# Optimization experiments

Hardware: AMD Instinct MI355X
Metric: run time of the kernel (lower is better)

## Reference

```python
import jax, jax.numpy as jnp
import numpy as np

BINS = 100
ALPHA = 0.1

def entropy_batch(h):
    # Faithful to torch: histogram path is detached (done in numpy in original).
    h = jax.lax.stop_gradient(h)
    B, D = h.shape
    hp = h - jnp.min(h, axis=1, keepdims=True)
    hn = hp / jnp.max(hp, axis=1, keepdims=True)  # normalized to [0, 1]
    # np.histogram with `bins` uniform bins over [0,1]; rightmost edge inclusive -> clip
    idx = jnp.clip(jnp.floor(hn * BINS).astype(jnp.int32), 0, BINS - 1)
    rows = jnp.arange(B)[:, None]
    counts = jnp.zeros((B, BINS), jnp.float32).at[rows, idx].add(1.0)
    px = counts / jnp.float32(D)
    safe = jnp.where(px > 0, px, 1.0)
    ent = -jnp.sum(px * jnp.log(safe), axis=1) + jnp.log(jnp.float32(BINS))
    return jnp.mean(ent)

def setup_inputs() -> dict:
    key = jax.random.key(0)
    ks = jax.random.split(key, 8)
    B = 65536
    archi = [246, 246, 246, 246, 246, 246]
    dims = [784] + archi
    inp = {"x": jax.random.normal(ks[0], (B, 1, 28, 28), jnp.float32)}
    for i in range(6):
        inp[f"W{i+1}"] = 0.01 * jax.random.normal(ks[i + 1], (dims[i + 1], dims[i]), jnp.float32)
        inp[f"b{i+1}"] = jnp.zeros((dims[i + 1],), jnp.float32)
    inp["W7"] = 0.01 * jax.random.normal(ks[7], (10, archi[-1]), jnp.float32)
    inp["b7"] = jnp.zeros((10,), jnp.float32)
    return inp

def reference(x, W1, b1, W2, b2, W3, b3, W4, b4, W5, b5, W6, b6, W7, b7):
    h = x.reshape(-1, 784)
    Hs = []
    for W, b in ((W1, b1), (W2, b2), (W3, b3), (W4, b4), (W5, b5), (W6, b6)):
        h = jax.nn.leaky_relu(h @ W.T + b, negative_slope=ALPHA)
        Hs.append(entropy_batch(h))
    logits = jax.nn.relu(h @ W7.T + b7)
    out = jax.nn.log_softmax(logits, axis=1)
    return (out, Hs[0], Hs[1], Hs[2], Hs[3], Hs[4], Hs[5])
```

## Files before the change

### kernel.cpp

```cpp
#include <hip/hip_runtime.h>
#include <cstdint>
#include <cmath>

#define BATCH 65536
#define NREAL 246
#define NPAD  256
#define K1    784
#define K1PAD 832
#define BINS  100
#define ALPHA 0.1f
#define RB    32
#define NBLK  (BATCH/RB)

typedef __bf16 bf16x8 __attribute__((ext_vector_type(8)));
typedef __bf16 bf16x4 __attribute__((ext_vector_type(4)));
typedef float  f32x4  __attribute__((ext_vector_type(4)));

#define OFF_HS     0
#define OFF_STAGE  16384
#define OFF_HIST   16384
#define OFF_MN     29184
#define OFF_MX     29696
#define OFF_LUT    30208
#define OFF_WENT   31232
#define LDS_TOTAL  31328

__global__ __launch_bounds__(256)
void pad_weights(const float* __restrict__ W1, const float* __restrict__ W2,
                 const float* __restrict__ W3, const float* __restrict__ W4,
                 const float* __restrict__ W5, const float* __restrict__ W6,
                 const float* __restrict__ W7,
                 const float* __restrict__ b1, const float* __restrict__ b2,
                 const float* __restrict__ b3, const float* __restrict__ b4,
                 const float* __restrict__ b5, const float* __restrict__ b6,
                 __bf16* __restrict__ W1p, __bf16* __restrict__ Wp,
                 __bf16* __restrict__ W7p, float* __restrict__ bpad)
{
    int tid = blockIdx.x * 256 + threadIdx.x;
    const int n1 = NPAD * K1PAD;
    const int n2 = 5 * NPAD * NPAD;
    const int n3 = 16 * NPAD;
    if (tid < n1) {
        int row = tid / K1PAD;
        int k   = tid - row * K1PAD;
        W1p[tid] = (__bf16)((row < NREAL && k < K1) ? W1[row * K1 + k] : 0.0f);
    } else if (tid < n1 + n2) {
        int t = tid - n1;
        int wsel = t >> 16;
        int idx  = t & 65535;
        int row  = idx >> 8, k = idx & 255;
        const float* W = (wsel == 0) ? W2 : (wsel == 1) ? W3 : (wsel == 2) ? W4
                        : (wsel == 3) ? W5 : W6;
        Wp[t] = (__bf16)((row < NREAL && k < NREAL) ? W[row * NREAL + k] : 0.0f);
    } else if (tid < n1 + n2 + n3) {
        int t = tid - n1 - n2;
        int row = t >> 8, k = t & 255;
        W7p[t] = (__bf16)((row < 10 && k < NREAL) ? W7[row * NREAL + k] : 0.0f);
    } else if (tid < n1 + n2 + n3 + 6 * NPAD) {
        int t = tid - n1 - n2 - n3;
        int li = t >> 8, k = t & 255;
        const float* b = (li == 0) ? b1 : (li == 1) ? b2 : (li == 2) ? b3
                        : (li == 3) ? b4 : (li == 4) ? b5 : b6;
        bpad[t] = (k < NREAL) ? b[k] : 0.0f;
    }
}

__global__ __launch_bounds__(256)
void mega(const float* __restrict__ x,
          const __bf16* __restrict__ W1p,
          const __bf16* __restrict__ Wp,
          const __bf16* __restrict__ W7p,
          const float* __restrict__ bpad,
          const float* __restrict__ b7,
          float* __restrict__ out, float* __restrict__ partial)
{
    __shared__ char smem[LDS_TOTAL];
    char*  Hb    = smem + OFF_HS;
    float* rowmn = (float*)(smem + OFF_MN);
    float* rowmx = (float*)(smem + OFF_MX);
    float* lut   = (float*)(smem + OFF_LUT);
    float* went  = (float*)(smem + OFF_WENT);
    int*   hist  = (int*)(smem + OFF_HIST);

    const int tid = threadIdx.x;
    const int w = tid >> 6, l = tid & 63;
    const int lane16 = l & 15, lane4 = l >> 4;
    const int m0 = blockIdx.x * RB;

    if (tid > 0 && tid < 247) lut[tid] = (float)tid * logf((float)tid);
    if (tid == 0) lut[0] = 0.0f;

    f32x4 acc[2][4];
#pragma unroll
    for (int i = 0; i < 2; ++i)
#pragma unroll
        for (int j = 0; j < 4; ++j) acc[i][j] = f32x4{0.f, 0.f, 0.f, 0.f};

    auto loadBh = [&](bf16x8 (&dst)[4], const __bf16* Bbase, int Kb, int kt, int kk) {
        const __bf16* p = Bbase + (size_t)(w * 64 + lane16) * Kb + kt * 64 + kk * 32 + lane4 * 8;
#pragma unroll
        for (int j = 0; j < 4; ++j)
            dst[j] = *(const bf16x8*)(p + (size_t)j * 16 * Kb);
    };

    auto computeHalf = [&](const char* Ab, int rowStride, int kbyte, const bf16x8 (&bfr)[4]) {
#pragma unroll
        for (int i = 0; i < 2; ++i) {
            int row = i * 16 + lane16;
            bf16x8 af = *(const bf16x8*)(Ab + row * rowStride + ((kbyte + lane4 * 16) ^ ((row & 7) << 4)));
            __builtin_amdgcn_s_setprio(1);
#pragma unroll
            for (int j = 0; j < 4; ++j)
                acc[i][j] = __builtin_amdgcn_mfma_f32_16x16x32_bf16(bfr[j], af, acc[i][j], 0, 0, 0);
            __builtin_amdgcn_s_setprio(0);
        }
    };

    auto epilogue = [&](const float* bp) {
        f32x4 bq[4];
#pragma unroll
        for (int j = 0; j < 4; ++j)
            bq[j] = *(const f32x4*)(bp + w * 64 + j * 16 + lane4 * 4);
#pragma unroll
        for (int i = 0; i < 2; ++i) {
            const int m = i * 16 + lane16;
            const int swz = (m & 7) << 4;
            float mn = 1e30f, mx = -1e30f;
#pragma unroll
            for (int j = 0; j < 4; ++j) {
                const int nbase = w * 64 + j * 16 + lane4 * 4;
                bf16x4 hv;
#pragma unroll
                for (int r = 0; r < 4; ++r) {
                    float v = acc[i][j][r] + bq[j][r];
                    v = v > 0.0f ? v : ALPHA * v;
                    bool valid = (nbase + r) < NREAL;
                    hv[r] = valid ? (__bf16)v : (__bf16)0.0f;
                    acc[i][j][r] = v;
                    mn = fminf(mn, valid ? v : 1e30f);
                    mx = fmaxf(mx, valid ? v : -1e30f);
                }
                *(bf16x4*)(Hb + m * 512 + ((nbase * 2) ^ swz)) = hv;
            }
            mn = fminf(mn, __shfl_xor(mn, 16, 64));
            mx = fmaxf(mx, __shfl_xor(mx, 16, 64));
            mn = fminf(mn, __shfl_xor(mn, 32, 64));
            mx = fmaxf(mx, __shfl_xor(mx, 32, 64));
            if (lane4 == 0) {
                rowmn[m * 4 + w] = mn;
                rowmx[m * 4 + w] = mx;
            }
        }
    };

    auto ezero = [&]() {
        int4* hz = (int4*)hist;
        const int4 z = int4{0, 0, 0, 0};
        hz[tid] = z; hz[tid + 256] = z; hz[tid + 512] = z;
        if (tid < 32) hz[tid + 768] = z;
    };
    auto efill = [&]() {
#pragma unroll
        for (int i = 0; i < 2; ++i) {
            const int m = i * 16 + lane16;
            f32x4 m4 = *(const f32x4*)(rowmn + m * 4);
            f32x4 x4 = *(const f32x4*)(rowmx + m * 4);
            float mn = fminf(fminf(m4[0], m4[1]), fminf(m4[2], m4[3]));
            float mx = fmaxf(fmaxf(x4[0], x4[1]), fmaxf(x4[2], x4[3]));
            float rgv = mx - mn;
            float rs = (rgv > 0.0f) ? 100.0f / rgv : 0.0f;
            int* hrow = hist + m * 100;
#pragma unroll
            for (int j = 0; j < 4; ++j) {
                const int nbase = w * 64 + j * 16 + lane4 * 4;
#pragma unroll
                for (int r = 0; r < 4; ++r) {
                    if (nbase + r < NREAL) {
                        int idx = (int)floorf((acc[i][j][r] - mn) * rs);
                        idx = idx < 0 ? 0 : (idx > BINS - 1 ? BINS - 1 : idx);
                        atomicAdd(&hrow[idx], 1);
                    }
                }
            }
        }
    };
    auto esum = [&](int li) {
        const int rg = l >> 3, q = l & 7;
        const int row = w * 8 + rg;
        float S = 0.0f;
#pragma unroll
        for (int t = 0; t < 13; ++t) {
            int b = q * 13 + t;
            if (b < 100) S += lut[hist[row * 100 + b]];
        }
#pragma unroll
        for (int off = 1; off < 64; off <<= 1) S += __shfl_xor(S, off, 64);
        if (l == 0) went[w * 6 + li] = 8.0f * logf(246.0f) - S * (1.0f / 246.0f);
    };

    bf16x8 curB[4], nxtB[4];

    {
        const int srow = tid >> 3;
        const int skc  = (tid & 7) * 8;
        float4 xr0, xr1;
        auto issueX = [&](int kt) {
            int k0 = kt * 64 + skc;
            if (k0 < K1) {
                const float* gx = x + (size_t)(m0 + srow) * K1 + k0;
                xr0 = *(const float4*)gx;
                xr1 = *(const float4*)(gx + 4);
            } else {
                xr0 = float4{0.f,0.f,0.f,0.f};
                xr1 = float4{0.f,0.f,0.f,0.f};
            }
        };
        auto writeX = [&](int buf) {
            bf16x8 h;
            h[0]=(__bf16)xr0.x; h[1]=(__bf16)xr0.y; h[2]=(__bf16)xr0.z; h[3]=(__bf16)xr0.w;
            h[4]=(__bf16)xr1.x; h[5]=(__bf16)xr1.y; h[6]=(__bf16)xr1.z; h[7]=(__bf16)xr1.w;
            char* st = smem + OFF_STAGE + buf * 4096;
            *(bf16x8*)(st + srow * 128 + ((skc * 2) ^ ((srow & 7) << 4))) = h;
        };

        issueX(0);
        writeX(0);
        issueX(1);
        loadBh(curB, W1p, K1PAD, 0, 0);
        for (int kt = 0; kt < 13; ++kt) {
            __syncthreads();
            if (kt < 12) {
                writeX((kt + 1) & 1);
                if (kt < 11) issueX(kt + 2);
            }
            const char* st = smem + OFF_STAGE + (kt & 1) * 4096;
            loadBh(nxtB, W1p, K1PAD, kt, 1);
            computeHalf(st, 128, 0, curB);
            if (kt < 12) loadBh(curB, W1p, K1PAD, kt + 1, 0);
            computeHalf(st, 128, 64, nxtB);
        }
    }

    loadBh(curB, Wp, NPAD, 0, 0);
    epilogue(bpad);
    __syncthreads();
    ezero();
    __syncthreads();
    efill();
    __syncthreads();
    esum(0);

    for (int li = 0; li < 5; ++li) {
        const __bf16* Bp = Wp + (size_t)li * (NPAD * NPAD);
#pragma unroll
        for (int i = 0; i < 2; ++i)
#pragma unroll
            for (int j = 0; j < 4; ++j) acc[i][j] = f32x4{0.f, 0.f, 0.f, 0.f};

#pragma unroll
        for (int kt = 0; kt < 4; ++kt) {
            loadBh(nxtB, Bp, NPAD, kt, 1);
            computeHalf(Hb, 512, kt * 128, curB);
            if (kt < 3)      loadBh(curB, Bp, NPAD, kt + 1, 0);
            else if (li < 4) loadBh(curB, Bp + NPAD * NPAD, NPAD, 0, 0);
            computeHalf(Hb, 512, kt * 128 + 64, nxtB);
        }

        __syncthreads();
        ezero();
        epilogue(bpad + (li + 1) * NPAD);
        __syncthreads();
        efill();
        __syncthreads();
        esum(li + 1);
    }

    if (w < 2) {
        f32x4 hacc = f32x4{0.f, 0.f, 0.f, 0.f};
        int row = w * 16 + lane16;
#pragma unroll
        for (int kt = 0; kt < 8; ++kt) {
            bf16x8 af = *(const bf16x8*)(Hb + row * 512 + ((kt * 64 + lane4 * 16) ^ ((row & 7) << 4)));
            bf16x8 bf = *(const bf16x8*)(W7p + (size_t)lane16 * NPAD + kt * 32 + lane4 * 8);
            hacc = __builtin_amdgcn_mfma_f32_16x16x32_bf16(af, bf, hacc, 0, 0, 0);
        }
        float bv = (lane16 < 10) ? b7[lane16] : 0.0f;
#pragma unroll
        for (int r = 0; r < 4; ++r) {
            float lg = fmaxf(hacc[r] + bv, 0.0f);
            float vm = (lane16 < 10) ? lg : -1e30f;
#pragma unroll
            for (int off = 8; off; off >>= 1) vm = fmaxf(vm, __shfl_xor(vm, off, 64));
            float ex = (lane16 < 10) ? expf(lg - vm) : 0.0f;
#pragma unroll
            for (int off = 8; off; off >>= 1) ex += __shfl_xor(ex, off, 64);
            float ls = vm + logf(ex);
            if (lane16 < 10) {
                int grow = m0 + w * 16 + lane4 * 4 + r;
                out[(size_t)grow * 10 + lane16] = lg - ls;
            }
        }
    }

    __syncthreads();
    if (tid < 6) {
        float s = 0.0f;
#pragma unroll
        for (int q = 0; q < 4; ++q) s += went[q * 6 + tid];
        partial[tid * NBLK + blockIdx.x] = s;
    }
}

__global__ __launch_bounds__(256)
void reduce_kernel(const float* __restrict__ partial, float* __restrict__ out)
{
    __shared__ float s[256];
    const int li = blockIdx.x, tid = threadIdx.x;
    float a = 0.0f;
    for (int i = tid; i < NBLK; i += 256) a += partial[li * NBLK + i];
    s[tid] = a;
    __syncthreads();
    for (int st = 128; st; st >>= 1) {
        if (tid < st) s[tid] += s[tid + st];
        __syncthreads();
    }
    if (tid == 0)
        out[(size_t)BATCH * 10 + li] = s[0] / (float)BATCH + logf((float)BINS);
}

extern "C" void kernel_launch(void* const* d_in, const int* in_sizes, int n_in,
                              void* d_out, int out_size, void* d_ws, size_t ws_size,
                              hipStream_t stream)
{
    (void)in_sizes; (void)n_in; (void)out_size; (void)ws_size;

    const float* x  = (const float*)d_in[0];
    const float* W1 = (const float*)d_in[1];
    const float* b1 = (const float*)d_in[2];
    const float* W2 = (const float*)d_in[3];
    const float* b2 = (const float*)d_in[4];
    const float* W3 = (const float*)d_in[5];
    const float* b3 = (const float*)d_in[6];
    const float* W4 = (const float*)d_in[7];
    const float* b4 = (const float*)d_in[8];
    const float* W5 = (const float*)d_in[9];
    const float* b5 = (const float*)d_in[10];
    const float* W6 = (const float*)d_in[11];
    const float* b6 = (const float*)d_in[12];
    const float* W7 = (const float*)d_in[13];
    const float* b7 = (const float*)d_in[14];

    char* ws = (char*)d_ws;
    __bf16* W1p = (__bf16*)(ws);
    __bf16* Wp  = (__bf16*)(ws + 425984);
    __bf16* W7p = (__bf16*)(ws + 1081344);
    float*  bpad = (float*)(ws + 1089536);
    float*  partial = (float*)(ws + 1095680);
    float*  out = (float*)d_out;

    pad_weights<<<2134, 256, 0, stream>>>(W1, W2, W3, W4, W5, W6, W7,
                                          b1, b2, b3, b4, b5, b6,
                                          W1p, Wp, W7p, bpad);
    mega<<<NBLK, 256, 0, stream>>>(x, W1p, Wp, W7p, bpad, b7, out, partial);
    reduce_kernel<<<6, 256, 0, stream>>>(partial, out);
}
```

Before: 297.3 us.

## Double rows per block and preload full layer weights into registers

Doubles the batch rows per block from 32 to 64, so each wave's weight fragments are reused across four row tiles instead of two. For the hidden layers it loads all of a layer's B fragments into registers (Ball[8][4]) up front, replacing the per-k double buffering, and prefetches the next layer's weights after the current GEMM. Layer 1 uses ping-pong register sets. This roughly doubles LDS use and greatly raises register pressure, which may reduce occupancy or cause spills.

```diff
diff --git a/kernel.cpp b/kernel.cpp
--- a/kernel.cpp
+++ b/kernel.cpp
@@ -9,7 +9,7 @@
 #define K1PAD 832
 #define BINS  100
 #define ALPHA 0.1f
-#define RB    32
+#define RB    64
 #define NBLK  (BATCH/RB)
 
 typedef __bf16 bf16x8 __attribute__((ext_vector_type(8)));
@@ -17,13 +17,13 @@
 typedef float  f32x4  __attribute__((ext_vector_type(4)));
 
 #define OFF_HS     0
-#define OFF_STAGE  16384
-#define OFF_HIST   16384
-#define OFF_MN     29184
-#define OFF_MX     29696
-#define OFF_LUT    30208
-#define OFF_WENT   31232
-#define LDS_TOTAL  31328
+#define OFF_STAGE  32768
+#define OFF_HIST   32768
+#define OFF_MN     58368
+#define OFF_MX     59392
+#define OFF_LUT    60416
+#define OFF_WENT   61440
+#define LDS_TOTAL  61568
 
 __global__ __launch_bounds__(256)
 void pad_weights(const float* __restrict__ W1, const float* __restrict__ W2,
@@ -87,31 +87,40 @@
     const int lane16 = l & 15, lane4 = l >> 4;
     const int m0 = blockIdx.x * RB;
 
-    if (tid > 0 && tid < 247) lut[tid] = (float)tid * logf((float)tid);
-    if (tid == 0) lut[0] = 0.0f;
-
-    f32x4 acc[2][4];
-#pragma unroll
-    for (int i = 0; i < 2; ++i)
+    if (tid < 247) lut[tid] = (tid > 0) ? (float)tid * logf((float)tid) : 0.0f;
+
+    f32x4 acc[4][4];
+#pragma unroll
+    for (int i = 0; i < 4; ++i)
 #pragma unroll
         for (int j = 0; j < 4; ++j) acc[i][j] = f32x4{0.f, 0.f, 0.f, 0.f};
 
-    auto loadBh = [&](bf16x8 (&dst)[4], const __bf16* Bbase, int Kb, int kt, int kk) {
-        const __bf16* p = Bbase + (size_t)(w * 64 + lane16) * Kb + kt * 64 + kk * 32 + lane4 * 8;
-#pragma unroll
-        for (int j = 0; j < 4; ++j)
-            dst[j] = *(const bf16x8*)(p + (size_t)j * 16 * Kb);
-    };
-
-    auto computeHalf = [&](const char* Ab, int rowStride, int kbyte, const bf16x8 (&bfr)[4]) {
-#pragma unroll
-        for (int i = 0; i < 2; ++i) {
-            int row = i * 16 + lane16;
-            bf16x8 af = *(const bf16x8*)(Ab + row * rowStride + ((kbyte + lane4 * 16) ^ ((row & 7) << 4)));
+    bf16x8 Ball[8][4];
+
+    auto loadAll = [&](const __bf16* Bbase) {
+        const __bf16* p = Bbase + (size_t)(w * 64 + lane16) * NPAD + lane4 * 8;
+#pragma unroll
+        for (int h = 0; h < 8; ++h)
+#pragma unroll
+            for (int j = 0; j < 4; ++j)
+                Ball[h][j] = *(const bf16x8*)(p + j * 16 * NPAD + h * 32);
+    };
+
+    auto gemmMid = [&]() {
+#pragma unroll
+        for (int h = 0; h < 8; ++h) {
+            bf16x8 af[4];
+#pragma unroll
+            for (int i = 0; i < 4; ++i) {
+                int m = i * 16 + lane16;
+                af[i] = *(const bf16x8*)(Hb + m * 512 + ((h * 64 + lane4 * 16) ^ ((m & 7) << 4)));
+            }
             __builtin_amdgcn_s_setprio(1);
 #pragma unroll
-            for (int j = 0; j < 4; ++j)
-                acc[i][j] = __builtin_amdgcn_mfma_f32_16x16x32_bf16(bfr[j], af, acc[i][j], 0, 0, 0);
+            for (int i = 0; i < 4; ++i)
+#pragma unroll
+                for (int j = 0; j < 4; ++j)
+                    acc[i][j] = __builtin_amdgcn_mfma_f32_16x16x32_bf16(Ball[h][j], af[i], acc[i][j], 0, 0, 0);
             __builtin_amdgcn_s_setprio(0);
         }
     };
@@ -122,7 +131,7 @@
         for (int j = 0; j < 4; ++j)
             bq[j] = *(const f32x4*)(bp + w * 64 + j * 16 + lane4 * 4);
 #pragma unroll
-        for (int i = 0; i < 2; ++i) {
+        for (int i = 0; i < 4; ++i) {
             const int m = i * 16 + lane16;
             const int swz = (m & 7) << 4;
             float mn = 1e30f, mx = -1e30f;
@@ -146,27 +155,26 @@
             mx = fmaxf(mx, __shfl_xor(mx, 16, 64));
             mn = fminf(mn, __shfl_xor(mn, 32, 64));
             mx = fmaxf(mx, __shfl_xor(mx, 32, 64));
-            if (lane4 == 0) {
-                rowmn[m * 4 + w] = mn;
-                rowmx[m * 4 + w] = mx;
-            }
+            if (lane4 == 0) { rowmn[m * 4 + w] = mn; rowmx[m * 4 + w] = mx; }
         }
     };
 
     auto ezero = [&]() {
         int4* hz = (int4*)hist;
         const int4 z = int4{0, 0, 0, 0};
-        hz[tid] = z; hz[tid + 256] = z; hz[tid + 512] = z;
-        if (tid < 32) hz[tid + 768] = z;
-    };
+#pragma unroll
+        for (int t = 0; t < 6; ++t) hz[tid + t * 256] = z;
+        if (tid < 64) hz[1536 + tid] = z;
+    };
+
     auto efill = [&]() {
 #pragma unroll
-        for (int i = 0; i < 2; ++i) {
+        for (int i = 0; i < 4; ++i) {
             const int m = i * 16 + lane16;
             f32x4 m4 = *(const f32x4*)(rowmn + m * 4);
-            f32x4 x4 = *(const f32x4*)(rowmx + m * 4);
+            f32x4 x4v = *(const f32x4*)(rowmx + m * 4);
             float mn = fminf(fminf(m4[0], m4[1]), fminf(m4[2], m4[3]));
-            float mx = fmaxf(fmaxf(x4[0], x4[1]), fmaxf(x4[2], x4[3]));
+            float mx = fmaxf(fmaxf(x4v[0], x4v[1]), fmaxf(x4v[2], x4v[3]));
             float rgv = mx - mn;
             float rs = (rgv > 0.0f) ? 100.0f / rgv : 0.0f;
             int* hrow = hist + m * 100;
@@ -184,64 +192,86 @@
             }
         }
     };
+
     auto esum = [&](int li) {
-        const int rg = l >> 3, q = l & 7;
-        const int row = w * 8 + rg;
+        const int rg = l >> 2, q = l & 3;
+        const int row = w * 16 + rg;
+        const int* hrow = hist + row * 100 + q * 25;
         float S = 0.0f;
 #pragma unroll
-        for (int t = 0; t < 13; ++t) {
-            int b = q * 13 + t;
-            if (b < 100) S += lut[hist[row * 100 + b]];
-        }
+        for (int t = 0; t < 25; ++t) S += lut[hrow[t]];
 #pragma unroll
         for (int off = 1; off < 64; off <<= 1) S += __shfl_xor(S, off, 64);
-        if (l == 0) went[w * 6 + li] = 8.0f * logf(246.0f) - S * (1.0f / 246.0f);
-    };
-
-    bf16x8 curB[4], nxtB[4];
+        if (l == 0) went[w * 6 + li] = 16.0f * logf(246.0f) - S * (1.0f / 246.0f);
+    };
 
     {
-        const int srow = tid >> 3;
-        const int skc  = (tid & 7) * 8;
-        float4 xr0, xr1;
+        const int srow = tid >> 2;
+        const int skq  = tid & 3;
+        float4 xr[4];
         auto issueX = [&](int kt) {
-            int k0 = kt * 64 + skc;
+            int k0 = kt * 64 + skq * 16;
             if (k0 < K1) {
                 const float* gx = x + (size_t)(m0 + srow) * K1 + k0;
-                xr0 = *(const float4*)gx;
-                xr1 = *(const float4*)(gx + 4);
+#pragma unroll
+                for (int q = 0; q < 4; ++q) xr[q] = *(const float4*)(gx + q * 4);
             } else {
-                xr0 = float4{0.f,0.f,0.f,0.f};
-                xr1 = float4{0.f,0.f,0.f,0.f};
+#pragma unroll
+                for (int q = 0; q < 4; ++q) xr[q] = float4{0.f, 0.f, 0.f, 0.f};
             }
         };
         auto writeX = [&](int buf) {
-            bf16x8 h;
-            h[0]=(__bf16)xr0.x; h[1]=(__bf16)xr0.y; h[2]=(__bf16)xr0.z; h[3]=(__bf16)xr0.w;
-            h[4]=(__bf16)xr1.x; h[5]=(__bf16)xr1.y; h[6]=(__bf16)xr1.z; h[7]=(__bf16)xr1.w;
-            char* st = smem + OFF_STAGE + buf * 4096;
-            *(bf16x8*)(st + srow * 128 + ((skc * 2) ^ ((srow & 7) << 4))) = h;
+            bf16x8 h0, h1;
+            h0[0]=(__bf16)xr[0].x; h0[1]=(__bf16)xr[0].y; h0[2]=(__bf16)xr[0].z; h0[3]=(__bf16)xr[0].w;
+            h0[4]=(__bf16)xr[1].x; h0[5]=(__bf16)xr[1].y; h0[6]=(__bf16)xr[1].z; h0[7]=(__bf16)xr[1].w;
+            h1[0]=(__bf16)xr[2].x; h1[1]=(__bf16)xr[2].y; h1[2]=(__bf16)xr[2].z; h1[3]=(__bf16)xr[2].w;
+            h1[4]=(__bf16)xr[3].x; h1[5]=(__bf16)xr[3].y; h1[6]=(__bf16)xr[3].z; h1[7]=(__bf16)xr[3].w;
+            char* st = smem + OFF_STAGE + buf * 8192;
+            const int swz = (srow & 7) << 4;
+            *(bf16x8*)(st + srow * 128 + ((skq * 32)      ^ swz)) = h0;
+            *(bf16x8*)(st + srow * 128 + ((skq * 32 + 16) ^ swz)) = h1;
         };
 
-        issueX(0);
-        writeX(0);
-        issueX(1);
-        loadBh(curB, W1p, K1PAD, 0, 0);
+        bf16x8 A0[4], A1[4], B0[4], B1[4];
+        auto loadKt = [&](bf16x8 (&C0)[4], bf16x8 (&C1)[4], int kt) {
+            const __bf16* p = W1p + (size_t)(w * 64 + lane16) * K1PAD + kt * 64 + lane4 * 8;
+#pragma unroll
+            for (int j = 0; j < 4; ++j) {
+                C0[j] = *(const bf16x8*)(p + (size_t)j * 16 * K1PAD);
+                C1[j] = *(const bf16x8*)(p + (size_t)j * 16 * K1PAD + 32);
+            }
+        };
+        auto l1c = [&](const char* st, const bf16x8 (&C0)[4], const bf16x8 (&C1)[4]) {
+#pragma unroll
+            for (int kk = 0; kk < 2; ++kk) {
+                bf16x8 af[4];
+#pragma unroll
+                for (int i = 0; i < 4; ++i) {
+                    int m = i * 16 + lane16;
+                    af[i] = *(const bf16x8*)(st + m * 128 + ((kk * 64 + lane4 * 16) ^ ((m & 7) << 4)));
+                }
+                __builtin_amdgcn_s_setprio(1);
+#pragma unroll
+                for (int i = 0; i < 4; ++i)
+#pragma unroll
+                    for (int j = 0; j < 4; ++j)
+                        acc[i][j] = __builtin_amdgcn_mfma_f32_16x16x32_bf16(kk ? C1[j] : C0[j], af[i], acc[i][j], 0, 0, 0);
+                __builtin_amdgcn_s_setprio(0);
+            }
+        };
+
+        issueX(0); writeX(0); issueX(1);
+        loadKt(A0, A1, 0);
         for (int kt = 0; kt < 13; ++kt) {
             __syncthreads();
-            if (kt < 12) {
-                writeX((kt + 1) & 1);
-                if (kt < 11) issueX(kt + 2);
-            }
-            const char* st = smem + OFF_STAGE + (kt & 1) * 4096;
-            loadBh(nxtB, W1p, K1PAD, kt, 1);
-            computeHalf(st, 128, 0, curB);
-            if (kt < 12) loadBh(curB, W1p, K1PAD, kt + 1, 0);
-            computeHalf(st, 128, 64, nxtB);
-        }
-    }
-
-    loadBh(curB, Wp, NPAD, 0, 0);
+            if (kt < 12) { writeX((kt + 1) & 1); if (kt < 11) issueX(kt + 2); }
+            const char* st = smem + OFF_STAGE + (kt & 1) * 8192;
+            if ((kt & 1) == 0) { if (kt < 12) loadKt(B0, B1, kt + 1); l1c(st, A0, A1); }
+            else               { if (kt < 12) loadKt(A0, A1, kt + 1); l1c(st, B0, B1); }
+        }
+    }
+
+    loadAll(Wp);
     epilogue(bpad);
     __syncthreads();
     ezero();
@@ -251,20 +281,13 @@
     esum(0);
 
     for (int li = 0; li < 5; ++li) {
-        const __bf16* Bp = Wp + (size_t)li * (NPAD * NPAD);
-#pragma unroll
-        for (int i = 0; i < 2; ++i)
+#pragma unroll
+        for (int i = 0; i < 4; ++i)
 #pragma unroll
             for (int j = 0; j < 4; ++j) acc[i][j] = f32x4{0.f, 0.f, 0.f, 0.f};
 
-#pragma unroll
-        for (int kt = 0; kt < 4; ++kt) {
-            loadBh(nxtB, Bp, NPAD, kt, 1);
-            computeHalf(Hb, 512, kt * 128, curB);
-            if (kt < 3)      loadBh(curB, Bp, NPAD, kt + 1, 0);
-            else if (li < 4) loadBh(curB, Bp + NPAD * NPAD, NPAD, 0, 0);
-            computeHalf(Hb, 512, kt * 128 + 64, nxtB);
-        }
+        gemmMid();
+        if (li < 4) loadAll(Wp + (size_t)(li + 1) * NPAD * NPAD);
 
         __syncthreads();
         ezero();
@@ -275,7 +298,7 @@
         esum(li + 1);
     }
 
-    if (w < 2) {
+    {
         f32x4 hacc = f32x4{0.f, 0.f, 0.f, 0.f};
         int row = w * 16 + lane16;
 #pragma unroll
@@ -304,9 +327,7 @@
 
     __syncthreads();
     if (tid < 6) {
-        float s = 0.0f;
-#pragma unroll
-        for (int q = 0; q < 4; ++q) s += went[q * 6 + tid];
+        float s = went[tid] + went[6 + tid] + went[12 + tid] + went[18 + tid];
         partial[tid * NBLK + blockIdx.x] = s;
     }
 }
```

New measurement: 289.9 us. -2.5%, faster.

## Interleave histogram entropy of previous layer with next layer's MFMA loop

Applied to the files above, without the earlier changes.

Moves the histogram fill for layer p into the K-loop of layer p+1's GEMM. Each wave bins its own 8 rows, reading the bf16 activations back from LDS and accumulating into a per-wave histogram region. The B-operand prefetch becomes a 3-deep register ring, and two block barriers per layer are removed. The histogram now uses bf16-rounded activations for min, max and binning rather than fp32 values, which can shift bin boundaries slightly. It also raises register pressure from the extra B buffers.

```diff
diff --git a/kernel.cpp b/kernel.cpp
--- a/kernel.cpp
+++ b/kernel.cpp
@@ -23,7 +23,7 @@
 #define OFF_MX     29696
 #define OFF_LUT    30208
 #define OFF_WENT   31232
-#define LDS_TOTAL  31328
+#define LDS_TOTAL  31360
 
 __global__ __launch_bounds__(256)
 void pad_weights(const float* __restrict__ W1, const float* __restrict__ W2,
@@ -87,8 +87,12 @@
     const int lane16 = l & 15, lane4 = l >> 4;
     const int m0 = blockIdx.x * RB;
 
-    if (tid > 0 && tid < 247) lut[tid] = (float)tid * logf((float)tid);
-    if (tid == 0) lut[0] = 0.0f;
+    const int rg = l >> 3, q = l & 7;
+    const int erow = w * 8 + rg;
+    const int eswz = (erow & 7) << 4;
+    int* histW = hist + w * 800;
+
+    if (tid < 247) lut[tid] = (tid > 0) ? (float)tid * logf((float)tid) : 0.0f;
 
     f32x4 acc[2][4];
 #pragma unroll
@@ -96,24 +100,13 @@
 #pragma unroll
         for (int j = 0; j < 4; ++j) acc[i][j] = f32x4{0.f, 0.f, 0.f, 0.f};
 
-    auto loadBh = [&](bf16x8 (&dst)[4], const __bf16* Bbase, int Kb, int kt, int kk) {
-        const __bf16* p = Bbase + (size_t)(w * 64 + lane16) * Kb + kt * 64 + kk * 32 + lane4 * 8;
+    bf16x8 Bq[3][4];
+
+    auto loadBq = [&](int s, const __bf16* Bbase, int hh) {
+        const __bf16* pp = Bbase + (size_t)(w * 64 + lane16) * NPAD + (hh >> 1) * 64 + (hh & 1) * 32 + lane4 * 8;
 #pragma unroll
         for (int j = 0; j < 4; ++j)
-            dst[j] = *(const bf16x8*)(p + (size_t)j * 16 * Kb);
-    };
-
-    auto computeHalf = [&](const char* Ab, int rowStride, int kbyte, const bf16x8 (&bfr)[4]) {
-#pragma unroll
-        for (int i = 0; i < 2; ++i) {
-            int row = i * 16 + lane16;
-            bf16x8 af = *(const bf16x8*)(Ab + row * rowStride + ((kbyte + lane4 * 16) ^ ((row & 7) << 4)));
-            __builtin_amdgcn_s_setprio(1);
-#pragma unroll
-            for (int j = 0; j < 4; ++j)
-                acc[i][j] = __builtin_amdgcn_mfma_f32_16x16x32_bf16(bfr[j], af, acc[i][j], 0, 0, 0);
-            __builtin_amdgcn_s_setprio(0);
-        }
+            Bq[s][j] = *(const bf16x8*)(pp + (size_t)j * 16 * NPAD);
     };
 
     auto epilogue = [&](const float* bp) {
@@ -136,9 +129,9 @@
                     v = v > 0.0f ? v : ALPHA * v;
                     bool valid = (nbase + r) < NREAL;
                     hv[r] = valid ? (__bf16)v : (__bf16)0.0f;
-                    acc[i][j][r] = v;
-                    mn = fminf(mn, valid ? v : 1e30f);
-                    mx = fmaxf(mx, valid ? v : -1e30f);
+                    float vb = (float)hv[r];
+                    mn = fminf(mn, valid ? vb : 1e30f);
+                    mx = fmaxf(mx, valid ? vb : -1e30f);
                 }
                 *(bf16x4*)(Hb + m * 512 + ((nbase * 2) ^ swz)) = hv;
             }
@@ -146,59 +139,22 @@
             mx = fmaxf(mx, __shfl_xor(mx, 16, 64));
             mn = fminf(mn, __shfl_xor(mn, 32, 64));
             mx = fmaxf(mx, __shfl_xor(mx, 32, 64));
-            if (lane4 == 0) {
-                rowmn[m * 4 + w] = mn;
-                rowmx[m * 4 + w] = mx;
-            }
+            if (lane4 == 0) { rowmn[m * 4 + w] = mn; rowmx[m * 4 + w] = mx; }
         }
     };
 
-    auto ezero = [&]() {
-        int4* hz = (int4*)hist;
-        const int4 z = int4{0, 0, 0, 0};
-        hz[tid] = z; hz[tid + 256] = z; hz[tid + 512] = z;
-        if (tid < 32) hz[tid + 768] = z;
-    };
-    auto efill = [&]() {
-#pragma unroll
-        for (int i = 0; i < 2; ++i) {
-            const int m = i * 16 + lane16;
-            f32x4 m4 = *(const f32x4*)(rowmn + m * 4);
-            f32x4 x4 = *(const f32x4*)(rowmx + m * 4);
-            float mn = fminf(fminf(m4[0], m4[1]), fminf(m4[2], m4[3]));
-            float mx = fmaxf(fmaxf(x4[0], x4[1]), fmaxf(x4[2], x4[3]));
-            float rgv = mx - mn;
-            float rs = (rgv > 0.0f) ? 100.0f / rgv : 0.0f;
-            int* hrow = hist + m * 100;
-#pragma unroll
-            for (int j = 0; j < 4; ++j) {
-                const int nbase = w * 64 + j * 16 + lane4 * 4;
-#pragma unroll
-                for (int r = 0; r < 4; ++r) {
-                    if (nbase + r < NREAL) {
-                        int idx = (int)floorf((acc[i][j][r] - mn) * rs);
-                        idx = idx < 0 ? 0 : (idx > BINS - 1 ? BINS - 1 : idx);
-                        atomicAdd(&hrow[idx], 1);
-                    }
-                }
-            }
-        }
-    };
     auto esum = [&](int li) {
-        const int rg = l >> 3, q = l & 7;
-        const int row = w * 8 + rg;
         float S = 0.0f;
+        const int* hrow = histW + rg * 100;
 #pragma unroll
         for (int t = 0; t < 13; ++t) {
             int b = q * 13 + t;
-            if (b < 100) S += lut[hist[row * 100 + b]];
+            if (b < 100) S += lut[hrow[b]];
         }
 #pragma unroll
         for (int off = 1; off < 64; off <<= 1) S += __shfl_xor(S, off, 64);
         if (l == 0) went[w * 6 + li] = 8.0f * logf(246.0f) - S * (1.0f / 246.0f);
     };
-
-    bf16x8 curB[4], nxtB[4];
 
     {
         const int srow = tid >> 3;
@@ -222,57 +178,121 @@
             char* st = smem + OFF_STAGE + buf * 4096;
             *(bf16x8*)(st + srow * 128 + ((skc * 2) ^ ((srow & 7) << 4))) = h;
         };
-
-        issueX(0);
-        writeX(0);
-        issueX(1);
-        loadBh(curB, W1p, K1PAD, 0, 0);
+        auto lB = [&](bf16x8 (&dst)[4], int kt, int kk) {
+            const __bf16* p = W1p + (size_t)(w * 64 + lane16) * K1PAD + kt * 64 + kk * 32 + lane4 * 8;
+#pragma unroll
+            for (int j = 0; j < 4; ++j)
+                dst[j] = *(const bf16x8*)(p + (size_t)j * 16 * K1PAD);
+        };
+        auto cH = [&](const char* st, int kbyte, const bf16x8 (&bfr)[4]) {
+#pragma unroll
+            for (int i = 0; i < 2; ++i) {
+                int m = i * 16 + lane16;
+                bf16x8 af = *(const bf16x8*)(st + m * 128 + ((kbyte + lane4 * 16) ^ ((m & 7) << 4)));
+                __builtin_amdgcn_s_setprio(1);
+#pragma unroll
+                for (int j = 0; j < 4; ++j)
+                    acc[i][j] = __builtin_amdgcn_mfma_f32_16x16x32_bf16(bfr[j], af, acc[i][j], 0, 0, 0);
+                __builtin_amdgcn_s_setprio(0);
+            }
+        };
+
+        bf16x8 curB[4], nxtB[4];
+        issueX(0); writeX(0); issueX(1);
+        lB(curB, 0, 0);
         for (int kt = 0; kt < 13; ++kt) {
             __syncthreads();
-            if (kt < 12) {
-                writeX((kt + 1) & 1);
-                if (kt < 11) issueX(kt + 2);
-            }
+            if (kt < 12) { writeX((kt + 1) & 1); if (kt < 11) issueX(kt + 2); }
             const char* st = smem + OFF_STAGE + (kt & 1) * 4096;
-            loadBh(nxtB, W1p, K1PAD, kt, 1);
-            computeHalf(st, 128, 0, curB);
-            if (kt < 12) loadBh(curB, W1p, K1PAD, kt + 1, 0);
-            computeHalf(st, 128, 64, nxtB);
-        }
-    }
-
-    loadBh(curB, Wp, NPAD, 0, 0);
+            lB(nxtB, kt, 1);
+            cH(st, 0, curB);
+            if (kt < 12) lB(curB, kt + 1, 0);
+            cH(st, 64, nxtB);
+        }
+    }
+
+    loadBq(0, Wp, 0);
+    loadBq(1, Wp, 1);
     epilogue(bpad);
     __syncthreads();
-    ezero();
-    __syncthreads();
-    efill();
-    __syncthreads();
-    esum(0);
-
-    for (int li = 0; li < 5; ++li) {
-        const __bf16* Bp = Wp + (size_t)li * (NPAD * NPAD);
+
+    for (int p = 0; p < 5; ++p) {
+        const __bf16* WpP = Wp + (size_t)p * (NPAD * NPAD);
+        const __bf16* WpN = WpP + NPAD * NPAD;
+
 #pragma unroll
         for (int i = 0; i < 2; ++i)
 #pragma unroll
             for (int j = 0; j < 4; ++j) acc[i][j] = f32x4{0.f, 0.f, 0.f, 0.f};
 
 #pragma unroll
-        for (int kt = 0; kt < 4; ++kt) {
-            loadBh(nxtB, Bp, NPAD, kt, 1);
-            computeHalf(Hb, 512, kt * 128, curB);
-            if (kt < 3)      loadBh(curB, Bp, NPAD, kt + 1, 0);
-            else if (li < 4) loadBh(curB, Bp + NPAD * NPAD, NPAD, 0, 0);
-            computeHalf(Hb, 512, kt * 128 + 64, nxtB);
-        }
+        for (int t = 0; t < 13; ++t) { int b = t * 64 + l; if (b < 800) histW[b] = 0; }
+        f32x4 m4 = *(const f32x4*)(rowmn + erow * 4);
+        f32x4 x4 = *(const f32x4*)(rowmx + erow * 4);
+        float emn = fminf(fminf(m4[0], m4[1]), fminf(m4[2], m4[3]));
+        float emx = fmaxf(fmaxf(x4[0], x4[1]), fmaxf(x4[2], x4[3]));
+        float ers = (emx > emn) ? 100.0f / (emx - emn) : 0.0f;
+        asm volatile("s_waitcnt lgkmcnt(0)" ::: "memory");
+
+#pragma unroll
+        for (int h = 0; h < 8; ++h) {
+            if (h < 6)      loadBq((h + 2) % 3, WpP, h + 2);
+            else if (p < 4) loadBq(h - 6, WpN, h - 6);
+#pragma unroll
+            for (int i = 0; i < 2; ++i) {
+                int m = i * 16 + lane16;
+                bf16x8 af = *(const bf16x8*)(Hb + m * 512 + ((h * 64 + lane4 * 16) ^ ((m & 7) << 4)));
+                __builtin_amdgcn_s_setprio(1);
+#pragma unroll
+                for (int j = 0; j < 4; ++j)
+                    acc[i][j] = __builtin_amdgcn_mfma_f32_16x16x32_bf16(Bq[h % 3][j], af, acc[i][j], 0, 0, 0);
+                __builtin_amdgcn_s_setprio(0);
+            }
+            {
+                int c0 = q * 32 + h * 4;
+                bf16x4 hv = *(const bf16x4*)(Hb + erow * 512 + ((c0 * 2) ^ eswz));
+#pragma unroll
+                for (int e = 0; e < 4; ++e) {
+                    if (c0 + e < NREAL) {
+                        int idx = (int)floorf(((float)hv[e] - emn) * ers);
+                        idx = idx < 0 ? 0 : (idx > BINS - 1 ? BINS - 1 : idx);
+                        atomicAdd(&histW[rg * 100 + idx], 1);
+                    }
+                }
+            }
+        }
+        asm volatile("s_waitcnt lgkmcnt(0)" ::: "memory");
+        esum(p);
 
         __syncthreads();
-        ezero();
-        epilogue(bpad + (li + 1) * NPAD);
+        epilogue(bpad + (size_t)(p + 1) * NPAD);
         __syncthreads();
-        efill();
-        __syncthreads();
-        esum(li + 1);
+    }
+
+    {
+#pragma unroll
+        for (int t = 0; t < 13; ++t) { int b = t * 64 + l; if (b < 800) histW[b] = 0; }
+        f32x4 m4 = *(const f32x4*)(rowmn + erow * 4);
+        f32x4 x4 = *(const f32x4*)(rowmx + erow * 4);
+        float emn = fminf(fminf(m4[0], m4[1]), fminf(m4[2], m4[3]));
+        float emx = fmaxf(fmaxf(x4[0], x4[1]), fmaxf(x4[2], x4[3]));
+        float ers = (emx > emn) ? 100.0f / (emx - emn) : 0.0f;
+        asm volatile("s_waitcnt lgkmcnt(0)" ::: "memory");
+#pragma unroll
+        for (int h = 0; h < 8; ++h) {
+            int c0 = q * 32 + h * 4;
+            bf16x4 hv = *(const bf16x4*)(Hb + erow * 512 + ((c0 * 2) ^ eswz));
+#pragma unroll
+            for (int e = 0; e < 4; ++e) {
+                if (c0 + e < NREAL) {
+                    int idx = (int)floorf(((float)hv[e] - emn) * ers);
+                    idx = idx < 0 ? 0 : (idx > BINS - 1 ? BINS - 1 : idx);
+                    atomicAdd(&histW[rg * 100 + idx], 1);
+                }
+            }
+        }
+        asm volatile("s_waitcnt lgkmcnt(0)" ::: "memory");
+        esum(5);
     }
 
     if (w < 2) {
@@ -304,9 +324,7 @@
 
     __syncthreads();
     if (tid < 6) {
-        float s = 0.0f;
-#pragma unroll
-        for (int q = 0; q < 4; ++q) s += went[q * 6 + tid];
+        float s = went[tid] + went[6 + tid] + went[12 + tid] + went[18 + tid];
         partial[tid * NBLK + blockIdx.x] = s;
     }
 }
```

Measured after the change: 295.4 us. No clear change (-0.6%).
